# Kernel optimization log

Measured on AMD Instinct MI355X. Metric: run time of the kernel, lower is better.

Reference implementation:

```python
import jax, jax.numpy as jnp
import numpy as np

B, C, Q, D = 64, 512, 64, 256  # D = 2 * hidden_size; similarity weight has 3*D = 768 entries


def _length_mask(key, batch, seqlen):
    # realistic padding masks: each row has a random valid prefix length in [seqlen//2, seqlen]
    lens = jax.random.randint(key, (batch,), seqlen // 2, seqlen + 1)
    return (jnp.arange(seqlen)[None, :] < lens[:, None]).astype(jnp.int32)


def setup_inputs() -> dict:
    key = jax.random.key(0)
    k1, k2, k3, k4, k5 = jax.random.split(key, 5)
    context = jax.random.normal(k1, (B, C, D), dtype=jnp.float32)
    question = jax.random.normal(k2, (B, Q, D), dtype=jnp.float32)
    context_mask = _length_mask(k3, B, C)
    question_mask = _length_mask(k4, B, Q)
    w = jax.random.normal(k5, (3 * D,), dtype=jnp.float32) * (1.0 / np.sqrt(3 * D))
    return {"context": context, "question": question,
            "context_mask": context_mask, "question_mask": question_mask, "w": w}


def reference(context, question, context_mask, question_mask, w):
    d = context.shape[-1]
    # Linear([c, q, c*q]) with no bias decomposes exactly into three terms.
    w_c, w_q, w_m = w[:d], w[d:2 * d], w[2 * d:]
    sim = ((context @ w_c)[:, :, None]                      # [B, C, 1]
           + (question @ w_q)[:, None, :]                   # [B, 1, Q]
           + jnp.einsum('bcd,bqd->bcq', context * w_m, question))  # [B, C, Q]
    neg = jnp.finfo(sim.dtype).min
    # context-to-query attention (mask question positions)
    sim_q = jnp.where(question_mask[:, None, :] != 0, sim, neg)
    a = jax.nn.softmax(sim_q, axis=2)                        # [B, C, Q]
    c2q = jnp.einsum('bcq,bqd->bcd', a, question)            # [B, C, D]
    # query-to-context attention (max over Q, mask context positions)
    sim_max = jnp.max(sim, axis=2)                           # [B, C]
    sim_max = jnp.where(context_mask != 0, sim_max, neg)
    b = jax.nn.softmax(sim_max, axis=1)                      # [B, C]
    q2c = jnp.einsum('bc,bcd->bd', b, context)[:, None, :]   # [B, 1, D]
    q2c = jnp.broadcast_to(q2c, context.shape)               # [B, C, D]
    g = jnp.concatenate([context, c2q, context * c2q, context * q2c], axis=-1)
    return g
```

## Files before the change

### kernel.cpp

```cpp
#include <hip/hip_runtime.h>
#include <hip/hip_bf16.h>
#include <float.h>

#define B_ 64
#define C_ 512
#define Q_ 64
#define D_ 256

typedef _Float16 f16x8 __attribute__((ext_vector_type(8)));
typedef float f32x4 __attribute__((ext_vector_type(4)));

union U4H8 { uint4 u; f16x8 h; };
union UH2 { _Float16 h[2]; uint32_t u; };

__device__ __forceinline__ uint32_t packh2(float a, float b) {
  UH2 v; v.h[0] = (_Float16)a; v.h[1] = (_Float16)b; return v.u;
}

__device__ __forceinline__ float wred_sum(float v) {
#pragma unroll
  for (int off = 32; off > 0; off >>= 1) v += __shfl_xor(v, off, 64);
  return v;
}
__device__ __forceinline__ float wred_max(float v) {
#pragma unroll
  for (int off = 32; off > 0; off >>= 1) v = fmaxf(v, __shfl_xor(v, off, 64));
  return v;
}

__global__ __launch_bounds__(256) void k_rowdot(const float* __restrict__ src,
                                                const float* __restrict__ wgt,
                                                float* __restrict__ out, int nrows) {
  int wv = threadIdx.x >> 6, ln = threadIdx.x & 63;
  int row = blockIdx.x * 4 + wv;
  if (row >= nrows) return;
  float4 s4 = *(const float4*)(src + (size_t)row * D_ + 4 * ln);
  float4 w4 = *(const float4*)(wgt + 4 * ln);
  float p = s4.x * w4.x + s4.y * w4.y + s4.z * w4.z + s4.w * w4.w;
  p = wred_sum(p);
  if (ln == 0) out[row] = p;
}

__global__ __launch_bounds__(256, 2) void k_main(
    const float* __restrict__ ctx, const float* __restrict__ qst,
    const int* __restrict__ qmask, const float* __restrict__ w,
    const float* __restrict__ qwq_g, float* __restrict__ g,
    float* __restrict__ simmax_g) {
  __shared__ __align__(16) ushort qraw[Q_ * D_];
  __shared__ __align__(16) ushort qT[D_ * Q_];
  __shared__ __align__(16) ushort pbuf[4][16 * Q_];
  __shared__ float qwq_l[Q_];
  __shared__ int   qml_l[Q_];

  const int bid = blockIdx.x;
  const int b = bid & 63;
  const int c0 = (bid >> 6) * 64;
  const int t = threadIdx.x;
  const int wv = t >> 6, ln = t & 63;
  const int lc = ln & 15;
  const int lg = ln >> 4;
  const int c0w = c0 + wv * 16;

  f16x8 bfrag[8];
  float cwc_p = 0.f;
  const float* crow = ctx + ((size_t)b * C_ + c0w + lc) * D_;
  float* grow0 = g + ((size_t)b * C_ + c0w + lc) * (4 * D_);
#pragma unroll
  for (int kk = 0; kk < 8; ++kk) {
    int kb = kk * 32 + lg * 8;
    float4 cv0 = *(const float4*)(crow + kb);
    float4 cv1 = *(const float4*)(crow + kb + 4);
    float4 wc0 = *(const float4*)(w + kb);
    float4 wc1 = *(const float4*)(w + kb + 4);
    float4 wm0 = *(const float4*)(w + 2 * D_ + kb);
    float4 wm1 = *(const float4*)(w + 2 * D_ + kb + 4);
    cwc_p += cv0.x * wc0.x + cv0.y * wc0.y + cv0.z * wc0.z + cv0.w * wc0.w
           + cv1.x * wc1.x + cv1.y * wc1.y + cv1.z * wc1.z + cv1.w * wc1.w;
    bfrag[kk][0] = (_Float16)(cv0.x * wm0.x);
    bfrag[kk][1] = (_Float16)(cv0.y * wm0.y);
    bfrag[kk][2] = (_Float16)(cv0.z * wm0.z);
    bfrag[kk][3] = (_Float16)(cv0.w * wm0.w);
    bfrag[kk][4] = (_Float16)(cv1.x * wm1.x);
    bfrag[kk][5] = (_Float16)(cv1.y * wm1.y);
    bfrag[kk][6] = (_Float16)(cv1.z * wm1.z);
    bfrag[kk][7] = (_Float16)(cv1.w * wm1.w);
    *(float4*)(grow0 + kb) = cv0;
    *(float4*)(grow0 + kb + 4) = cv1;
  }
  float cwc = cwc_p;
  cwc += __shfl_xor(cwc, 16, 64);
  cwc += __shfl_xor(cwc, 32, 64);

  const float* qb = qst + (size_t)b * Q_ * D_;
#pragma unroll 4
  for (int it = 0; it < 32; ++it) {
    int idx = it * 256 + t;
    int q = idx >> 7, jp = idx & 127;
    float2 v = *(const float2*)(qb + q * D_ + 2 * jp);
    int ch = jp >> 2;
    int phys = (ch & ~7) | ((ch & 7) ^ (q & 7));
    *(uint32_t*)((char*)qraw + q * 512 + phys * 16 + (jp & 3) * 4) = packh2(v.x, v.y);
  }
#pragma unroll 4
  for (int it = 0; it < 32; ++it) {
    int q = t & 63;
    int jp = (t >> 6) + 4 * it;
    float2 v = *(const float2*)(qb + q * D_ + 2 * jp);
    int d0 = 2 * jp, d1 = d0 + 1;
    UH2 h0; h0.h[0] = (_Float16)v.x;
    UH2 h1; h1.h[0] = (_Float16)v.y;
    *(ushort*)((char*)qT + d0 * 128 + (((q >> 3) ^ (d0 & 7)) << 4) + (q & 7) * 2) = (ushort)(h0.u & 0xffff);
    *(ushort*)((char*)qT + d1 * 128 + (((q >> 3) ^ (d1 & 7)) << 4) + (q & 7) * 2) = (ushort)(h1.u & 0xffff);
  }
  if (t < Q_) { qwq_l[t] = qwq_g[b * Q_ + t]; qml_l[t] = qmask[b * Q_ + t]; }
  __syncthreads();

  f32x4 sacc[4];
#pragma unroll
  for (int tq = 0; tq < 4; ++tq) sacc[tq] = f32x4{0.f, 0.f, 0.f, 0.f};
#pragma unroll
  for (int tq = 0; tq < 4; ++tq) {
    int q = 16 * tq + lc;
#pragma unroll
    for (int kk = 0; kk < 8; ++kk) {
      int ch = lg + 4 * kk;
      int phys = (ch & ~7) | ((ch & 7) ^ (q & 7));
      U4H8 a; a.u = *(const uint4*)((const char*)qraw + q * 512 + phys * 16);
      sacc[tq] = __builtin_amdgcn_mfma_f32_16x16x32_f16(a.h, bfrag[kk], sacc[tq], 0, 0, 0);
    }
  }

  float vals[4][4];
  float rmax = -FLT_MAX;
#pragma unroll
  for (int tq = 0; tq < 4; ++tq) {
    float4 qw4 = *(const float4*)(qwq_l + 16 * tq + 4 * lg);
#pragma unroll
    for (int r = 0; r < 4; ++r) {
      float qv = (r == 0) ? qw4.x : (r == 1) ? qw4.y : (r == 2) ? qw4.z : qw4.w;
      vals[tq][r] = sacc[tq][r] + cwc + qv;
      rmax = fmaxf(rmax, vals[tq][r]);
    }
  }
  rmax = fmaxf(rmax, __shfl_xor(rmax, 16, 64));
  rmax = fmaxf(rmax, __shfl_xor(rmax, 32, 64));
  if (ln < 16) simmax_g[b * C_ + c0w + lc] = rmax;

  float mmax = -FLT_MAX;
#pragma unroll
  for (int tq = 0; tq < 4; ++tq) {
    int4 qm4 = *(const int4*)(qml_l + 16 * tq + 4 * lg);
#pragma unroll
    for (int r = 0; r < 4; ++r) {
      int m = (r == 0) ? qm4.x : (r == 1) ? qm4.y : (r == 2) ? qm4.z : qm4.w;
      vals[tq][r] = m ? vals[tq][r] : -FLT_MAX;
      mmax = fmaxf(mmax, vals[tq][r]);
    }
  }
  mmax = fmaxf(mmax, __shfl_xor(mmax, 16, 64));
  mmax = fmaxf(mmax, __shfl_xor(mmax, 32, 64));
  float esum = 0.f;
#pragma unroll
  for (int tq = 0; tq < 4; ++tq)
#pragma unroll
    for (int r = 0; r < 4; ++r) {
      vals[tq][r] = __expf(vals[tq][r] - mmax);
      esum += vals[tq][r];
    }
  esum += __shfl_xor(esum, 16, 64);
  esum += __shfl_xor(esum, 32, 64);
  float inv = 1.f / esum;
#pragma unroll
  for (int tq = 0; tq < 4; ++tq) {
    uint32_t p01 = packh2(vals[tq][0] * inv, vals[tq][1] * inv);
    uint32_t p23 = packh2(vals[tq][2] * inv, vals[tq][3] * inv);
    int qb4 = 16 * tq + 4 * lg;
    int phys = ((qb4 >> 3) ^ (lc & 7));
    char* dst = (char*)pbuf[wv] + lc * 128 + phys * 16 + (qb4 & 7) * 2;
    *(uint2*)dst = uint2{p01, p23};
  }

  f16x8 pfrag[2];
#pragma unroll
  for (int ks = 0; ks < 2; ++ks) {
    int phys = (lg + 4 * ks) ^ (lc & 7);
    U4H8 a; a.u = *(const uint4*)((const char*)pbuf[wv] + lc * 128 + phys * 16);
    pfrag[ks] = a.h;
  }
  const float* crow2 = ctx + ((size_t)b * C_ + c0w) * D_;
  float* grow = g + ((size_t)b * C_ + c0w) * (4 * D_);
#pragma unroll 4
  for (int dt = 0; dt < 16; ++dt) {
    int d = dt * 16 + lc;
    f32x4 acc = f32x4{0.f, 0.f, 0.f, 0.f};
#pragma unroll
    for (int ks = 0; ks < 2; ++ks) {
      int phys = (lg + 4 * ks) ^ (d & 7);
      U4H8 bq; bq.u = *(const uint4*)((const char*)qT + d * 128 + phys * 16);
      acc = __builtin_amdgcn_mfma_f32_16x16x32_f16(pfrag[ks], bq.h, acc, 0, 0, 0);
    }
#pragma unroll
    for (int r = 0; r < 4; ++r) {
      int crel = 4 * lg + r;
      float cval = crow2[crel * D_ + d];
      size_t off = (size_t)crel * (4 * D_) + D_ + d;
      grow[off] = acc[r];
      grow[off + D_] = cval * acc[r];
    }
  }
}

__global__ __launch_bounds__(256) void k_bsoft(const float* __restrict__ simmax,
                                               const int* __restrict__ cmask,
                                               float* __restrict__ bl) {
  int b = blockIdx.x, t = threadIdx.x;
  int wv = t >> 6, ln = t & 63;
  float v0 = simmax[b * C_ + t], v1 = simmax[b * C_ + 256 + t];
  if (!cmask[b * C_ + t]) v0 = -FLT_MAX;
  if (!cmask[b * C_ + 256 + t]) v1 = -FLT_MAX;
  __shared__ float sred[4];
  __shared__ float ssum[4];
  float mx = wred_max(fmaxf(v0, v1));
  if (ln == 0) sred[wv] = mx;
  __syncthreads();
  float bm = fmaxf(fmaxf(sred[0], sred[1]), fmaxf(sred[2], sred[3]));
  float e0 = __expf(v0 - bm), e1 = __expf(v1 - bm);
  float ps = wred_sum(e0 + e1);
  if (ln == 0) ssum[wv] = ps;
  __syncthreads();
  float bs = ssum[0] + ssum[1] + ssum[2] + ssum[3];
  bl[b * C_ + t] = e0 / bs;
  bl[b * C_ + 256 + t] = e1 / bs;
}

__global__ __launch_bounds__(256) void k_q2c_part(const float* __restrict__ ctx,
                                                  const float* __restrict__ bl,
                                                  float* __restrict__ part) {
  int b = blockIdx.x, ch = blockIdx.y, t = threadIdx.x;
  float acc = 0.f;
  int cbeg = ch * 64;
#pragma unroll 4
  for (int c = cbeg; c < cbeg + 64; ++c)
    acc += bl[b * C_ + c] * ctx[((size_t)b * C_ + c) * D_ + t];
  part[((size_t)b * 8 + ch) * D_ + t] = acc;
}

__global__ __launch_bounds__(256) void k_q2c_sum(const float* __restrict__ part,
                                                 float* __restrict__ q2c) {
  int b = blockIdx.x, t = threadIdx.x;
  float s = 0.f;
#pragma unroll
  for (int ch = 0; ch < 8; ++ch) s += part[((size_t)b * 8 + ch) * D_ + t];
  q2c[b * D_ + t] = s;
}

__global__ __launch_bounds__(256) void k_g3(const float* __restrict__ ctx,
                                            const float* __restrict__ q2c,
                                            float* __restrict__ g) {
  size_t i = (size_t)blockIdx.x * 256 + threadIdx.x;
  int d4 = (int)(i & 63);
  size_t row = i >> 6;
  int b = (int)(row >> 9);
  float4 cv = *(const float4*)(ctx + row * D_ + 4 * d4);
  float4 qv = *(const float4*)(q2c + (size_t)b * D_ + 4 * d4);
  float4 o{cv.x * qv.x, cv.y * qv.y, cv.z * qv.z, cv.w * qv.w};
  *(float4*)(g + row * (4 * D_) + 3 * D_ + 4 * d4) = o;
}

extern "C" void kernel_launch(void* const* d_in, const int* in_sizes, int n_in,
                              void* d_out, int out_size, void* d_ws, size_t ws_size,
                              hipStream_t stream) {
  const float* ctx   = (const float*)d_in[0];
  const float* qst   = (const float*)d_in[1];
  const int*   cmask = (const int*)d_in[2];
  const int*   qmask = (const int*)d_in[3];
  const float* w     = (const float*)d_in[4];
  float* g  = (float*)d_out;
  float* ws = (float*)d_ws;

  float* qwq    = ws;
  float* simmax = ws + 4096;
  float* bl     = ws + 36864;
  float* part   = ws + 69632;
  float* q2c    = ws + 200704;

  k_rowdot<<<dim3(B_ * Q_ / 4), 256, 0, stream>>>(qst, w + D_, qwq, B_ * Q_);
  k_main<<<dim3(512), 256, 0, stream>>>(ctx, qst, qmask, w, qwq, g, simmax);
  k_bsoft<<<dim3(B_), 256, 0, stream>>>(simmax, cmask, bl);
  k_q2c_part<<<dim3(B_, 8), 256, 0, stream>>>(ctx, bl, part);
  k_q2c_sum<<<dim3(B_), 256, 0, stream>>>(part, q2c);
  k_g3<<<dim3(B_ * C_ * 64 / 256), 256, 0, stream>>>(ctx, q2c, g);
}
```

Before: 66.05 us.

## Share one LDS buffer for Q and Q-transpose, swap MFMA operands, fuse b-softmax

k_main now uses a single shared buffer: Q is staged row-major for the similarity MFMA, then, after a barrier, overwritten with the transposed Q for the c2q MFMA. This halves that LDS footprint so three blocks per CU can be resident. The c2q MFMA operands are swapped so each lane holds four consecutive d values of one context row, which allows float4 loads of context and float4 stores of the c2q and context*c2q outputs. The b-softmax kernel is folded into the q2c partial kernel, and each of the 8 chunk blocks recomputes the softmax redundantly in LDS, which removes one launch and the bl round trip at the cost of an extra barrier and a serialized Q transpose stage.

```diff
diff --git a/kernel.cpp b/kernel.cpp
--- a/kernel.cpp
+++ b/kernel.cpp
@@ -41,13 +41,12 @@
   if (ln == 0) out[row] = p;
 }
 
-__global__ __launch_bounds__(256, 2) void k_main(
+__global__ __launch_bounds__(256, 3) void k_main(
     const float* __restrict__ ctx, const float* __restrict__ qst,
     const int* __restrict__ qmask, const float* __restrict__ w,
     const float* __restrict__ qwq_g, float* __restrict__ g,
     float* __restrict__ simmax_g) {
-  __shared__ __align__(16) ushort qraw[Q_ * D_];
-  __shared__ __align__(16) ushort qT[D_ * Q_];
+  __shared__ __align__(16) ushort qbuf[Q_ * D_];
   __shared__ __align__(16) ushort pbuf[4][16 * Q_];
   __shared__ float qwq_l[Q_];
   __shared__ int   qml_l[Q_];
@@ -99,8 +98,77 @@
     float2 v = *(const float2*)(qb + q * D_ + 2 * jp);
     int ch = jp >> 2;
     int phys = (ch & ~7) | ((ch & 7) ^ (q & 7));
-    *(uint32_t*)((char*)qraw + q * 512 + phys * 16 + (jp & 3) * 4) = packh2(v.x, v.y);
-  }
+    *(uint32_t*)((char*)qbuf + q * 512 + phys * 16 + (jp & 3) * 4) = packh2(v.x, v.y);
+  }
+  if (t < Q_) { qwq_l[t] = qwq_g[b * Q_ + t]; qml_l[t] = qmask[b * Q_ + t]; }
+  __syncthreads();
+
+  f32x4 sacc[4];
+#pragma unroll
+  for (int tq = 0; tq < 4; ++tq) sacc[tq] = f32x4{0.f, 0.f, 0.f, 0.f};
+#pragma unroll
+  for (int tq = 0; tq < 4; ++tq) {
+    int q = 16 * tq + lc;
+#pragma unroll
+    for (int kk = 0; kk < 8; ++kk) {
+      int ch = lg + 4 * kk;
+      int phys = (ch & ~7) | ((ch & 7) ^ (q & 7));
+      U4H8 a; a.u = *(const uint4*)((const char*)qbuf + q * 512 + phys * 16);
+      sacc[tq] = __builtin_amdgcn_mfma_f32_16x16x32_f16(a.h, bfrag[kk], sacc[tq], 0, 0, 0);
+    }
+  }
+
+  float vals[4][4];
+  float rmax = -FLT_MAX;
+#pragma unroll
+  for (int tq = 0; tq < 4; ++tq) {
+    float4 qw4 = *(const float4*)(qwq_l + 16 * tq + 4 * lg);
+#pragma unroll
+    for (int r = 0; r < 4; ++r) {
+      float qv = (r == 0) ? qw4.x : (r == 1) ? qw4.y : (r == 2) ? qw4.z : qw4.w;
+      vals[tq][r] = sacc[tq][r] + cwc + qv;
+      rmax = fmaxf(rmax, vals[tq][r]);
+    }
+  }
+  rmax = fmaxf(rmax, __shfl_xor(rmax, 16, 64));
+  rmax = fmaxf(rmax, __shfl_xor(rmax, 32, 64));
+  if (ln < 16) simmax_g[b * C_ + c0w + lc] = rmax;
+
+  float mmax = -FLT_MAX;
+#pragma unroll
+  for (int tq = 0; tq < 4; ++tq) {
+    int4 qm4 = *(const int4*)(qml_l + 16 * tq + 4 * lg);
+#pragma unroll
+    for (int r = 0; r < 4; ++r) {
+      int m = (r == 0) ? qm4.x : (r == 1) ? qm4.y : (r == 2) ? qm4.z : qm4.w;
+      vals[tq][r] = m ? vals[tq][r] : -FLT_MAX;
+      mmax = fmaxf(mmax, vals[tq][r]);
+    }
+  }
+  mmax = fmaxf(mmax, __shfl_xor(mmax, 16, 64));
+  mmax = fmaxf(mmax, __shfl_xor(mmax, 32, 64));
+  float esum = 0.f;
+#pragma unroll
+  for (int tq = 0; tq < 4; ++tq)
+#pragma unroll
+    for (int r = 0; r < 4; ++r) {
+      vals[tq][r] = __expf(vals[tq][r] - mmax);
+      esum += vals[tq][r];
+    }
+  esum += __shfl_xor(esum, 16, 64);
+  esum += __shfl_xor(esum, 32, 64);
+  float inv = 1.f / esum;
+#pragma unroll
+  for (int tq = 0; tq < 4; ++tq) {
+    uint32_t p01 = packh2(vals[tq][0] * inv, vals[tq][1] * inv);
+    uint32_t p23 = packh2(vals[tq][2] * inv, vals[tq][3] * inv);
+    int qb4 = 16 * tq + 4 * lg;
+    int phys = ((qb4 >> 3) ^ (lc & 7));
+    char* dst = (char*)pbuf[wv] + lc * 128 + phys * 16 + (qb4 & 7) * 2;
+    *(uint2*)dst = uint2{p01, p23};
+  }
+  __syncthreads();
+
 #pragma unroll 4
   for (int it = 0; it < 32; ++it) {
     int q = t & 63;
@@ -109,117 +177,51 @@
     int d0 = 2 * jp, d1 = d0 + 1;
     UH2 h0; h0.h[0] = (_Float16)v.x;
     UH2 h1; h1.h[0] = (_Float16)v.y;
-    *(ushort*)((char*)qT + d0 * 128 + (((q >> 3) ^ (d0 & 7)) << 4) + (q & 7) * 2) = (ushort)(h0.u & 0xffff);
-    *(ushort*)((char*)qT + d1 * 128 + (((q >> 3) ^ (d1 & 7)) << 4) + (q & 7) * 2) = (ushort)(h1.u & 0xffff);
-  }
-  if (t < Q_) { qwq_l[t] = qwq_g[b * Q_ + t]; qml_l[t] = qmask[b * Q_ + t]; }
-  __syncthreads();
-
-  f32x4 sacc[4];
-#pragma unroll
-  for (int tq = 0; tq < 4; ++tq) sacc[tq] = f32x4{0.f, 0.f, 0.f, 0.f};
-#pragma unroll
-  for (int tq = 0; tq < 4; ++tq) {
-    int q = 16 * tq + lc;
-#pragma unroll
-    for (int kk = 0; kk < 8; ++kk) {
-      int ch = lg + 4 * kk;
-      int phys = (ch & ~7) | ((ch & 7) ^ (q & 7));
-      U4H8 a; a.u = *(const uint4*)((const char*)qraw + q * 512 + phys * 16);
-      sacc[tq] = __builtin_amdgcn_mfma_f32_16x16x32_f16(a.h, bfrag[kk], sacc[tq], 0, 0, 0);
-    }
-  }
-
-  float vals[4][4];
-  float rmax = -FLT_MAX;
-#pragma unroll
-  for (int tq = 0; tq < 4; ++tq) {
-    float4 qw4 = *(const float4*)(qwq_l + 16 * tq + 4 * lg);
-#pragma unroll
-    for (int r = 0; r < 4; ++r) {
-      float qv = (r == 0) ? qw4.x : (r == 1) ? qw4.y : (r == 2) ? qw4.z : qw4.w;
-      vals[tq][r] = sacc[tq][r] + cwc + qv;
-      rmax = fmaxf(rmax, vals[tq][r]);
-    }
-  }
-  rmax = fmaxf(rmax, __shfl_xor(rmax, 16, 64));
-  rmax = fmaxf(rmax, __shfl_xor(rmax, 32, 64));
-  if (ln < 16) simmax_g[b * C_ + c0w + lc] = rmax;
-
-  float mmax = -FLT_MAX;
-#pragma unroll
-  for (int tq = 0; tq < 4; ++tq) {
-    int4 qm4 = *(const int4*)(qml_l + 16 * tq + 4 * lg);
-#pragma unroll
-    for (int r = 0; r < 4; ++r) {
-      int m = (r == 0) ? qm4.x : (r == 1) ? qm4.y : (r == 2) ? qm4.z : qm4.w;
-      vals[tq][r] = m ? vals[tq][r] : -FLT_MAX;
-      mmax = fmaxf(mmax, vals[tq][r]);
-    }
-  }
-  mmax = fmaxf(mmax, __shfl_xor(mmax, 16, 64));
-  mmax = fmaxf(mmax, __shfl_xor(mmax, 32, 64));
-  float esum = 0.f;
-#pragma unroll
-  for (int tq = 0; tq < 4; ++tq)
-#pragma unroll
-    for (int r = 0; r < 4; ++r) {
-      vals[tq][r] = __expf(vals[tq][r] - mmax);
-      esum += vals[tq][r];
-    }
-  esum += __shfl_xor(esum, 16, 64);
-  esum += __shfl_xor(esum, 32, 64);
-  float inv = 1.f / esum;
-#pragma unroll
-  for (int tq = 0; tq < 4; ++tq) {
-    uint32_t p01 = packh2(vals[tq][0] * inv, vals[tq][1] * inv);
-    uint32_t p23 = packh2(vals[tq][2] * inv, vals[tq][3] * inv);
-    int qb4 = 16 * tq + 4 * lg;
-    int phys = ((qb4 >> 3) ^ (lc & 7));
-    char* dst = (char*)pbuf[wv] + lc * 128 + phys * 16 + (qb4 & 7) * 2;
-    *(uint2*)dst = uint2{p01, p23};
-  }
-
-  f16x8 pfrag[2];
+    *(ushort*)((char*)qbuf + d0 * 128 + (((q >> 3) ^ (d0 & 7)) << 4) + (q & 7) * 2) = (ushort)(h0.u & 0xffff);
+    *(ushort*)((char*)qbuf + d1 * 128 + (((q >> 3) ^ (d1 & 7)) << 4) + (q & 7) * 2) = (ushort)(h1.u & 0xffff);
+  }
+  __syncthreads();
+
+  f16x8 pfragB[2];
 #pragma unroll
   for (int ks = 0; ks < 2; ++ks) {
     int phys = (lg + 4 * ks) ^ (lc & 7);
     U4H8 a; a.u = *(const uint4*)((const char*)pbuf[wv] + lc * 128 + phys * 16);
-    pfrag[ks] = a.h;
-  }
-  const float* crow2 = ctx + ((size_t)b * C_ + c0w) * D_;
-  float* grow = g + ((size_t)b * C_ + c0w) * (4 * D_);
+    pfragB[ks] = a.h;
+  }
+  const float* crow2 = ctx + ((size_t)b * C_ + c0w + lc) * D_;
+  float* grow = g + ((size_t)b * C_ + c0w + lc) * (4 * D_);
 #pragma unroll 4
   for (int dt = 0; dt < 16; ++dt) {
-    int d = dt * 16 + lc;
     f32x4 acc = f32x4{0.f, 0.f, 0.f, 0.f};
 #pragma unroll
     for (int ks = 0; ks < 2; ++ks) {
+      int d = dt * 16 + lc;
       int phys = (lg + 4 * ks) ^ (d & 7);
-      U4H8 bq; bq.u = *(const uint4*)((const char*)qT + d * 128 + phys * 16);
-      acc = __builtin_amdgcn_mfma_f32_16x16x32_f16(pfrag[ks], bq.h, acc, 0, 0, 0);
-    }
-#pragma unroll
-    for (int r = 0; r < 4; ++r) {
-      int crel = 4 * lg + r;
-      float cval = crow2[crel * D_ + d];
-      size_t off = (size_t)crel * (4 * D_) + D_ + d;
-      grow[off] = acc[r];
-      grow[off + D_] = cval * acc[r];
-    }
-  }
-}
-
-__global__ __launch_bounds__(256) void k_bsoft(const float* __restrict__ simmax,
-                                               const int* __restrict__ cmask,
-                                               float* __restrict__ bl) {
-  int b = blockIdx.x, t = threadIdx.x;
+      U4H8 aq; aq.u = *(const uint4*)((const char*)qbuf + d * 128 + phys * 16);
+      acc = __builtin_amdgcn_mfma_f32_16x16x32_f16(aq.h, pfragB[ks], acc, 0, 0, 0);
+    }
+    int dcol = dt * 16 + 4 * lg;
+    float4 cvv = *(const float4*)(crow2 + dcol);
+    float4 c2qv{acc[0], acc[1], acc[2], acc[3]};
+    *(float4*)(grow + D_ + dcol) = c2qv;
+    float4 p2{cvv.x * c2qv.x, cvv.y * c2qv.y, cvv.z * c2qv.z, cvv.w * c2qv.w};
+    *(float4*)(grow + 2 * D_ + dcol) = p2;
+  }
+}
+
+__global__ __launch_bounds__(256) void k_q2c_bs(const float* __restrict__ ctx,
+                                                const float* __restrict__ simmax,
+                                                const int* __restrict__ cmask,
+                                                float* __restrict__ part) {
+  int b = blockIdx.x, ch = blockIdx.y, t = threadIdx.x;
   int wv = t >> 6, ln = t & 63;
+  __shared__ float bls[C_];
+  __shared__ float sred[4];
+  __shared__ float ssum[4];
   float v0 = simmax[b * C_ + t], v1 = simmax[b * C_ + 256 + t];
   if (!cmask[b * C_ + t]) v0 = -FLT_MAX;
   if (!cmask[b * C_ + 256 + t]) v1 = -FLT_MAX;
-  __shared__ float sred[4];
-  __shared__ float ssum[4];
   float mx = wred_max(fmaxf(v0, v1));
   if (ln == 0) sred[wv] = mx;
   __syncthreads();
@@ -229,19 +231,15 @@
   if (ln == 0) ssum[wv] = ps;
   __syncthreads();
   float bs = ssum[0] + ssum[1] + ssum[2] + ssum[3];
-  bl[b * C_ + t] = e0 / bs;
-  bl[b * C_ + 256 + t] = e1 / bs;
-}
-
-__global__ __launch_bounds__(256) void k_q2c_part(const float* __restrict__ ctx,
-                                                  const float* __restrict__ bl,
-                                                  float* __restrict__ part) {
-  int b = blockIdx.x, ch = blockIdx.y, t = threadIdx.x;
+  float invbs = 1.f / bs;
+  bls[t] = e0 * invbs;
+  bls[256 + t] = e1 * invbs;
+  __syncthreads();
   float acc = 0.f;
   int cbeg = ch * 64;
 #pragma unroll 4
   for (int c = cbeg; c < cbeg + 64; ++c)
-    acc += bl[b * C_ + c] * ctx[((size_t)b * C_ + c) * D_ + t];
+    acc += bls[c] * ctx[((size_t)b * C_ + c) * D_ + t];
   part[((size_t)b * 8 + ch) * D_ + t] = acc;
 }
 
@@ -280,14 +278,12 @@
 
   float* qwq    = ws;
   float* simmax = ws + 4096;
-  float* bl     = ws + 36864;
-  float* part   = ws + 69632;
-  float* q2c    = ws + 200704;
+  float* part   = ws + 36864;
+  float* q2c    = ws + 167936;
 
   k_rowdot<<<dim3(B_ * Q_ / 4), 256, 0, stream>>>(qst, w + D_, qwq, B_ * Q_);
   k_main<<<dim3(512), 256, 0, stream>>>(ctx, qst, qmask, w, qwq, g, simmax);
-  k_bsoft<<<dim3(B_), 256, 0, stream>>>(simmax, cmask, bl);
-  k_q2c_part<<<dim3(B_, 8), 256, 0, stream>>>(ctx, bl, part);
+  k_q2c_bs<<<dim3(B_, 8), 256, 0, stream>>>(ctx, simmax, cmask, part);
   k_q2c_sum<<<dim3(B_), 256, 0, stream>>>(part, q2c);
   k_g3<<<dim3(B_ * C_ * 64 / 256), 256, 0, stream>>>(ctx, q2c, g);
 }
```

Result: slower. 68.42 us (+3.6%).
